# Performance work log

Hardware: AMD Instinct MI355X
Metric: run time of the kernel (lower is better)

The kernel has to match this reference:

```python
import jax, jax.numpy as jnp
import numpy as np

H, HD, ROPE_BASE, E = 16, 64, 10000.0, 8
D, F = 1024, 2048


def layer_norm(x, g, b, eps=1e-5):
    mu = jnp.mean(x, axis=-1, keepdims=True)
    var = jnp.mean((x - mu) ** 2, axis=-1, keepdims=True)
    return (x - mu) * jax.lax.rsqrt(var + eps) * g + b


def apply_rotary(x, cos, sin):
    d = x.shape[-1]
    x1, x2 = x[..., : d // 2], x[..., d // 2:]
    return jnp.concatenate([x1 * cos - x2 * sin, x1 * sin + x2 * cos], axis=-1)


def setup_inputs() -> dict:
    key = jax.random.key(0)
    ks = jax.random.split(key, 8)
    B, T = 2, 2048
    x = jax.random.normal(ks[0], (B, T, D), jnp.float32)
    mask = jnp.triu(jnp.ones((T, T), bool), k=1)[None, None]  # True = masked (causal)
    s = 0.02
    return {
        "x": x,
        "mask": mask,
        "pos_offset": 0,
        "ln1_g": jnp.ones((D,), jnp.float32),
        "ln1_b": jnp.zeros((D,), jnp.float32),
        "qkv_w": jax.random.normal(ks[1], (D, 3 * H * HD), jnp.float32) * s,
        "qkv_b": jnp.zeros((3 * H * HD,), jnp.float32),
        "attn_out_w": jax.random.normal(ks[2], (H * HD, D), jnp.float32) * s,
        "attn_out_b": jnp.zeros((D,), jnp.float32),
        "ln2_g": jnp.ones((D,), jnp.float32),
        "ln2_b": jnp.zeros((D,), jnp.float32),
        "gate_w": jax.random.normal(ks[3], (D, E), jnp.float32) * s,
        "gate_b": jnp.zeros((E,), jnp.float32),
        "fc_w": jax.random.normal(ks[4], (E, D, 2 * F), jnp.float32) * s,
        "fc_b": jnp.zeros((E, 2 * F), jnp.float32),
        "eout_w": jax.random.normal(ks[5], (E, F, D), jnp.float32) * s,
        "eout_b": jnp.zeros((E, D), jnp.float32),
    }


def reference(x, mask, pos_offset, ln1_g, ln1_b, qkv_w, qkv_b, attn_out_w, attn_out_b,
              ln2_g, ln2_b, gate_w, gate_b, fc_w, fc_b, eout_w, eout_b):
    B, T, _ = x.shape
    # ---- Self-attention with inline RoPE ----
    h = layer_norm(x, ln1_g, ln1_b)
    qkv = h @ qkv_w + qkv_b  # [B,T,3*H*HD]
    q, k, v = jnp.split(qkv, 3, axis=-1)
    q, k, v = (t.reshape(B, T, H, HD).transpose(0, 2, 1, 3) for t in (q, k, v))  # [B,H,T,HD]
    inv_freq = 1.0 / ROPE_BASE ** (jnp.arange(0, HD, 2, dtype=jnp.float32) / HD)
    pos = (jnp.arange(T) + pos_offset).astype(jnp.float32)
    freqs = pos[:, None] * inv_freq[None, :]  # [T,HD/2]
    cos, sin = jnp.cos(freqs)[None, None], jnp.sin(freqs)[None, None]
    q = apply_rotary(q, cos, sin)
    k = apply_rotary(k, cos, sin)
    attn = jnp.einsum('bhqd,bhkd->bhqk', q, k) / (HD ** 0.5)
    attn = jnp.where(mask, -jnp.finfo(attn.dtype).max, attn)
    w = jax.nn.softmax(attn, axis=-1)
    o = jnp.einsum('bhqk,bhkd->bhqd', w, v).transpose(0, 2, 1, 3).reshape(B, T, H * HD)
    x = x + (o @ attn_out_w + attn_out_b)
    # ---- Dense soft-MoE GEGLU feed-forward ----
    h2 = layer_norm(x, ln2_g, ln2_b).reshape(-1, D)  # [N,D]
    gate_probs = jax.nn.softmax(h2 @ gate_w + gate_b, axis=-1)  # [N,E]
    fc = jnp.einsum('nd,edf->nef', h2, fc_w) + fc_b  # [N,E,2F]
    x1, x2 = jnp.split(fc, 2, axis=-1)
    act = x1 * jax.nn.gelu(x2, approximate=False)  # [N,E,F]
    expert_out = jnp.einsum('nef,efd->ned', act, eout_w) + eout_b  # [N,E,D]
    weighted = jnp.einsum('ned,ne->nd', expert_out, gate_probs)
    util = jnp.mean(gate_probs, axis=0)
    util_loss = jnp.sum((util - 1.0 / E) ** 2)
    return x + weighted.reshape(B, T, D), util_loss
```

## Files before the change

kernel.cpp:

```cpp
#include <hip/hip_runtime.h>
#include <hip/hip_bf16.h>

typedef __hip_bfloat16 bf16;
typedef short bf16x8 __attribute__((ext_vector_type(8)));
typedef float f32x4 __attribute__((ext_vector_type(4)));

__device__ __forceinline__ unsigned short f2bf(float f){
  __hip_bfloat16 h = __float2bfloat16(f);
  unsigned short u; __builtin_memcpy(&u, &h, 2); return u;
}

__device__ __forceinline__ void gload_lds16(const void* g, void* l){
  __builtin_amdgcn_global_load_lds((const __attribute__((address_space(1))) unsigned int*)g,
                                   (__attribute__((address_space(3))) unsigned int*)l, 16, 0, 0);
}

__device__ __forceinline__ float fast_gelu(float x){
  float t = 1.5957691216f * x * (1.f + 0.044715f * x * x);
  return x / (1.f + __expf(-t));
}


__global__ __launch_bounds__(256) void packT_kernel(const float* __restrict__ in, bf16* __restrict__ out, int R, int C){
  __shared__ float tile[32][33];
  const int tid = threadIdx.x;
  const int tc = tid & 31, tr = tid >> 5;
  const int r0 = blockIdx.y * 32, c0 = blockIdx.x * 32;
  #pragma unroll
  for (int i=0;i<4;i++)
    tile[tr + i*8][tc] = in[(size_t)(r0 + tr + i*8)*C + c0 + tc];
  __syncthreads();
  #pragma unroll
  for (int i=0;i<4;i++){
    int oc = tr + i*8;
    out[(size_t)(c0 + oc)*R + r0 + tc] = __float2bfloat16(tile[tc][oc]);
  }
}

__global__ __launch_bounds__(256) void pack_fc_kernel(const float* __restrict__ fcw, bf16* __restrict__ out){
  __shared__ float tile[32][33];
  const int tid = threadIdx.x;
  const int tc = tid & 31, tr = tid >> 5;
  const int e = blockIdx.z;
  const int d0 = blockIdx.y * 32, j0 = blockIdx.x * 32;
  #pragma unroll
  for (int i=0;i<4;i++)
    tile[tr + i*8][tc] = fcw[((size_t)e*1024 + d0 + tr + i*8)*4096 + j0 + tc];
  __syncthreads();
  #pragma unroll
  for (int i=0;i<4;i++){
    int j = j0 + tr + i*8;
    int cl = ((j & 2047) >> 4)*32 + (j >> 11)*16 + (j & 15);
    out[((size_t)e*4096 + cl)*1024 + d0 + tc] = __float2bfloat16(tile[tc][tr + i*8]);
  }
}

__global__ __launch_bounds__(256) void pack_eout_kernel(const float* __restrict__ eow, bf16* __restrict__ out){
  __shared__ float tile[32][33];
  const int tid = threadIdx.x;
  const int tc = tid & 31, tr = tid >> 5;
  const int e = blockIdx.z;
  const int d0 = blockIdx.y * 32, f0 = blockIdx.x * 32;
  #pragma unroll
  for (int i=0;i<4;i++)
    tile[tr + i*8][tc] = eow[((size_t)e*2048 + f0 + tr + i*8)*1024 + d0 + tc];
  __syncthreads();
  #pragma unroll
  for (int i=0;i<4;i++){
    int d = d0 + tr + i*8;
    out[(size_t)d*16384 + e*2048 + f0 + tc] = __float2bfloat16(tile[tc][tr + i*8]);
  }
}

__global__ __launch_bounds__(256) void pack_biasfc_kernel(const float* __restrict__ fcb, float* __restrict__ biasFc){
  int c = blockIdx.x*256 + threadIdx.x;
  int e = c >> 12, cl = c & 4095;
  int g = cl >> 5, w = cl & 31;
  int j = (w >> 4)*2048 + g*16 + (w & 15);
  biasFc[c] = fcb[e*4096 + j];
}


__global__ __launch_bounds__(256) void ln1_kernel(const float* __restrict__ x, const float* __restrict__ g,
                                                  const float* __restrict__ b, bf16* __restrict__ h){
  const int row = blockIdx.x, tid = threadIdx.x;
  const int lane = tid & 63, wave = tid >> 6;
  const float4 v = reinterpret_cast<const float4*>(x + (size_t)row*1024)[tid];
  float s1 = v.x + v.y + v.z + v.w;
  float s2 = v.x*v.x + v.y*v.y + v.z*v.z + v.w*v.w;
  #pragma unroll
  for (int off=1; off<64; off<<=1){ s1 += __shfl_xor(s1, off); s2 += __shfl_xor(s2, off); }
  __shared__ float rb[8];
  if (lane == 0){ rb[wave] = s1; rb[4+wave] = s2; }
  __syncthreads();
  s1 = rb[0]+rb[1]+rb[2]+rb[3];
  s2 = rb[4]+rb[5]+rb[6]+rb[7];
  const float mu = s1 * (1.f/1024.f);
  const float rst = rsqrtf(s2 * (1.f/1024.f) - mu*mu + 1e-5f);
  const float4 gg = reinterpret_cast<const float4*>(g)[tid];
  const float4 bb = reinterpret_cast<const float4*>(b)[tid];
  ushort4 st;
  st.x = f2bf((v.x-mu)*rst*gg.x + bb.x);
  st.y = f2bf((v.y-mu)*rst*gg.y + bb.y);
  st.z = f2bf((v.z-mu)*rst*gg.z + bb.z);
  st.w = f2bf((v.w-mu)*rst*gg.w + bb.w);
  reinterpret_cast<ushort4*>(h + (size_t)row*1024)[tid] = st;
}

__global__ __launch_bounds__(256) void ln2gate_kernel(const float* __restrict__ xr, const float* __restrict__ g,
    const float* __restrict__ b, const float* __restrict__ gw, const float* __restrict__ gb,
    bf16* __restrict__ h2, float* __restrict__ gate){
  const int row = blockIdx.x, tid = threadIdx.x;
  const int lane = tid & 63, wave = tid >> 6;
  const float4 v = reinterpret_cast<const float4*>(xr + (size_t)row*1024)[tid];
  float s1 = v.x+v.y+v.z+v.w, s2 = v.x*v.x+v.y*v.y+v.z*v.z+v.w*v.w;
  #pragma unroll
  for (int off=1; off<64; off<<=1){ s1 += __shfl_xor(s1, off); s2 += __shfl_xor(s2, off); }
  __shared__ float rb[8];
  if (lane == 0){ rb[wave] = s1; rb[4+wave] = s2; }
  __syncthreads();
  s1 = rb[0]+rb[1]+rb[2]+rb[3];
  s2 = rb[4]+rb[5]+rb[6]+rb[7];
  const float mu = s1*(1.f/1024.f);
  const float rst = rsqrtf(s2*(1.f/1024.f) - mu*mu + 1e-5f);
  const int c = tid*4;
  const float4 gg = reinterpret_cast<const float4*>(g)[tid];
  const float4 bb = reinterpret_cast<const float4*>(b)[tid];
  float nh[4];
  nh[0] = (v.x-mu)*rst*gg.x + bb.x;
  nh[1] = (v.y-mu)*rst*gg.y + bb.y;
  nh[2] = (v.z-mu)*rst*gg.z + bb.z;
  nh[3] = (v.w-mu)*rst*gg.w + bb.w;
  ushort4 st; st.x = f2bf(nh[0]); st.y = f2bf(nh[1]); st.z = f2bf(nh[2]); st.w = f2bf(nh[3]);
  reinterpret_cast<ushort4*>(h2 + (size_t)row*1024)[tid] = st;
  float gp[8];
  #pragma unroll
  for (int e=0;e<8;e++)
    gp[e] = nh[0]*gw[(c+0)*8+e] + nh[1]*gw[(c+1)*8+e] + nh[2]*gw[(c+2)*8+e] + nh[3]*gw[(c+3)*8+e];
  #pragma unroll
  for (int off=1; off<64; off<<=1)
    #pragma unroll
    for (int e=0;e<8;e++) gp[e] += __shfl_xor(gp[e], off);
  __shared__ float gbuf[4][8];
  if (lane == 0)
    #pragma unroll
    for (int e=0;e<8;e++) gbuf[wave][e] = gp[e];
  __syncthreads();
  if (tid == 0){
    float l[8], mx = -1e30f;
    #pragma unroll
    for (int e=0;e<8;e++){ l[e] = gbuf[0][e]+gbuf[1][e]+gbuf[2][e]+gbuf[3][e] + gb[e]; mx = fmaxf(mx, l[e]); }
    float se = 0.f;
    #pragma unroll
    for (int e=0;e<8;e++){ l[e] = __expf(l[e]-mx); se += l[e]; }
    const float inv = 1.f/se;
    #pragma unroll
    for (int e=0;e<8;e++) gate[row*8+e] = l[e]*inv;
  }
}

template<int EPI>
__global__ __launch_bounds__(256) void gemm_bt(
    const bf16* __restrict__ A, const bf16* __restrict__ BT,
    int N, int K, int kPerSlice,
    bf16* __restrict__ outb, float* __restrict__ outf,
    const float* __restrict__ bias, const float* __restrict__ resid,
    const float* __restrict__ gate)
{
  __shared__ __align__(16) bf16 As[128*32];
  __shared__ __align__(16) bf16 Bs[128*32];
  const int tid = threadIdx.x;
  const int lane = tid & 63, wave = tid >> 6;
  const int wr = wave >> 1, wc = wave & 1;
  const int lr = lane & 15, lg = lane >> 4;
  const int row0 = blockIdx.y * 128, col0 = blockIdx.x * 128;
  const int kstart = blockIdx.z * kPerSlice, kend = kstart + kPerSlice;

  const int swzA = lg ^ ((lr >> 1) & 3);

  f32x4 acc[4][4];
  #pragma unroll
  for (int i=0;i<4;i++)
    #pragma unroll
    for (int j=0;j<4;j++) acc[i][j] = (f32x4){0.f,0.f,0.f,0.f};

  for (int k0 = kstart; k0 < kend; k0 += 32){
    if (k0 != kstart) __syncthreads();
    #pragma unroll
    for (int i=0;i<2;i++){
      int ch = i*256 + tid;
      int r = ch >> 2, c = ch & 3;
      int cs = c ^ ((r >> 1) & 3);
      gload_lds16(A  + (size_t)(row0 + r)*K + k0 + cs*8, (void*)&As[ch*8]);
      gload_lds16(BT + (size_t)(col0 + r)*K + k0 + cs*8, (void*)&Bs[ch*8]);
    }
    __syncthreads();
    bf16x8 a[4], bfr[4];
    #pragma unroll
    for (int mi=0;mi<4;mi++) a[mi] = *reinterpret_cast<const bf16x8*>(&As[(wr*64 + mi*16 + lr)*32 + swzA*8]);
    #pragma unroll
    for (int ni=0;ni<4;ni++) bfr[ni] = *reinterpret_cast<const bf16x8*>(&Bs[(wc*64 + ni*16 + lr)*32 + swzA*8]);
    #pragma unroll
    for (int mi=0;mi<4;mi++)
      #pragma unroll
      for (int ni=0;ni<4;ni++)
        acc[mi][ni] = __builtin_amdgcn_mfma_f32_16x16x32_bf16(a[mi], bfr[ni], acc[mi][ni], 0,0,0);
  }

  const int rbase0 = row0 + wr*64;
  #pragma unroll
  for (int mi=0;mi<4;mi++){
    const int r4 = rbase0 + mi*16 + lg*4;
    #pragma unroll
    for (int ni=0;ni<4;ni++){
      const int c = col0 + wc*64 + ni*16 + lr;
      #pragma unroll
      for (int j=0;j<4;j++){
        const int rr = r4 + j;
        float v = acc[mi][ni][j];
        if (EPI == 0) outb[(size_t)rr*N + c] = __float2bfloat16(v + bias[c]);
        else outf[(size_t)rr*N + c] = v + bias[c] + resid[(size_t)rr*N + c];
      }
    }
  }
}

template<int EPI>
__global__ __launch_bounds__(512, 2) void gemm256(
    const bf16* __restrict__ A, const bf16* __restrict__ BT,
    int K, int kPerSlice,
    bf16* __restrict__ outb, float* __restrict__ outf,
    const float* __restrict__ bias, const float* __restrict__ gate)
{
  __shared__ __align__(16) bf16 lds[2][2][16384];
  const int tid = threadIdx.x;
  const int lane = tid & 63, wave = tid >> 6;
  const int wr = wave >> 2, wc = wave & 3;
  const int lr = lane & 15, lg = lane >> 4;
  const int row0 = blockIdx.y * 256, col0 = blockIdx.x * 256;
  const int kstart = blockIdx.z * kPerSlice;
  const int NT = kPerSlice >> 6;
  const int NITER = NT >> 1;

  f32x4 acc[8][4];
  #pragma unroll
  for (int i=0;i<8;i++)
    #pragma unroll
    for (int j=0;j<4;j++) acc[i][j] = (f32x4){0.f,0.f,0.f,0.f};

  auto stage = [&](int t, int ht){
    if (t >= NT) return;
    const bf16* gbase = (ht < 2) ? (A  + (size_t)(row0 + (ht&1)*128) * K)
                                 : (BT + (size_t)(col0 + (ht&1)*128) * K);
    const int k0 = kstart + t*64;
    bf16* dst = &lds[t&1][ht>>1][(ht&1)*8192];
    #pragma unroll
    for (int l=0;l<2;l++){
      const int c = tid + l*512;
      const int r = c >> 3, col16 = c & 7;
      const int cs = col16 ^ (r & 7);
      gload_lds16(gbase + (size_t)r*K + k0 + cs*8, (void*)&dst[c*8]);
    }
  };

  bf16x8 afr[4][2], bfr[4][2];
  auto rdA = [&](int mh, int buf){
    #pragma unroll
    for (int m2=0;m2<4;m2++)
      #pragma unroll
      for (int kk=0;kk<2;kk++){
        const int row = wr*128 + mh*64 + m2*16 + lr;
        afr[m2][kk] = *reinterpret_cast<const bf16x8*>(
            &lds[buf][0][row*64 + (((kk*4+lg) ^ (lr&7))*8)]);
      }
  };
  auto rdB = [&](int nh, int buf){
    #pragma unroll
    for (int n2=0;n2<2;n2++)
      #pragma unroll
      for (int kk=0;kk<2;kk++){
        const int row = wc*64 + (nh*2+n2)*16 + lr;
        bfr[nh*2+n2][kk] = *reinterpret_cast<const bf16x8*>(
            &lds[buf][1][row*64 + (((kk*4+lg) ^ (lr&7))*8)]);
      }
  };
  auto mfmaQ = [&](int mh, int nh){
    __builtin_amdgcn_s_setprio(1);
    #pragma unroll
    for (int m2=0;m2<4;m2++)
      #pragma unroll
      for (int n2=0;n2<2;n2++)
        #pragma unroll
        for (int kk=0;kk<2;kk++)
          acc[mh*4+m2][nh*2+n2] = __builtin_amdgcn_mfma_f32_16x16x32_bf16(
              afr[m2][kk], bfr[nh*2+n2][kk], acc[mh*4+m2][nh*2+n2], 0,0,0);
    __builtin_amdgcn_s_setprio(0);
  };

#define BAR()   __builtin_amdgcn_s_barrier()
#define LGKM0() do { asm volatile("s_waitcnt lgkmcnt(0)" ::: "memory"); \
                     __builtin_amdgcn_sched_barrier(0); } while(0)
#define VMC(n)  do { asm volatile("s_waitcnt vmcnt(" #n ")" ::: "memory"); \
                     __builtin_amdgcn_sched_barrier(0); } while(0)

  stage(0,0); stage(0,1); stage(0,2); stage(0,3); stage(1,0); stage(1,1);
  VMC(4);
  BAR();

  for (int it = 0; it < NITER; ++it){
    const int tB = it*2;
    const bool more = (it + 1 < NITER);

    stage(tB+1, 2); stage(tB+1, 3); rdA(0,0); rdB(0,0);
    LGKM0(); mfmaQ(0,0);
    rdB(1,0);
    LGKM0(); mfmaQ(0,1);
    rdA(1,0);
    LGKM0(); mfmaQ(1,0);
    BAR(); stage(tB+2, 0); stage(tB+2, 1); mfmaQ(1,1);
    if (more) { VMC(4); } else { VMC(0); }
    BAR();

    stage(tB+2, 2); stage(tB+2, 3); rdA(0,1); rdB(0,1);
    LGKM0(); mfmaQ(0,0);
    rdB(1,1);
    LGKM0(); mfmaQ(0,1);
    rdA(1,1);
    LGKM0(); mfmaQ(1,0);
    BAR(); stage(tB+3, 0); stage(tB+3, 1); mfmaQ(1,1);
    if (more) { VMC(4); } else { VMC(0); }
    BAR();
  }
#undef BAR
#undef LGKM0
#undef VMC

  #pragma unroll
  for (int mi=0;mi<8;mi++){
    const int r4 = row0 + wr*128 + mi*16 + lg*4;
    if (EPI == 2){
      #pragma unroll
      for (int p=0;p<2;p++){
        const int c1 = col0 + wc*64 + p*32 + lr;
        const int fg = (c1 >> 5)*16 + lr;
        const int e  = fg >> 11;
        const float b1 = bias[c1], b2 = bias[c1 + 16];
        #pragma unroll
        for (int j=0;j<4;j++){
          const int rr = r4 + j;
          const float x1v = acc[mi][2*p][j] + b1;
          const float x2v = acc[mi][2*p+1][j] + b2;
          const float gl = fast_gelu(x2v);
          outb[(size_t)rr*16384 + fg] = __float2bfloat16(x1v * gl * gate[rr*8 + e]);
        }
      }
    } else {
      #pragma unroll
      for (int ni=0;ni<4;ni++){
        const int c = col0 + wc*64 + ni*16 + lr;
        #pragma unroll
        for (int j=0;j<4;j++)
          outf[(size_t)blockIdx.z*4194304 + (size_t)(r4 + j)*1024 + c] = acc[mi][ni][j];
      }
    }
  }
}

__global__ __launch_bounds__(256) void rope_kernel(bf16* __restrict__ qkv, const int* __restrict__ posoff){
  const int idx = blockIdx.x*256 + threadIdx.x;
  const int i = idx & 31;
  const int h = (idx >> 5) & 15;
  const int n = idx >> 9;
  const float pos = (float)((n & 2047) + posoff[0]);
  const float ang = pos * __expf(-0.2878231366f * (float)i);
  float sn, cs;
  __sincosf(ang, &sn, &cs);
  size_t base = (size_t)n*3072 + h*64 + i;
  {
    float x1 = __bfloat162float(qkv[base]);
    float x2 = __bfloat162float(qkv[base + 32]);
    qkv[base]      = __float2bfloat16((x1*cs - x2*sn) * 0.125f);
    qkv[base + 32] = __float2bfloat16((x1*sn + x2*cs) * 0.125f);
  }
  {
    float x1 = __bfloat162float(qkv[base + 1024]);
    float x2 = __bfloat162float(qkv[base + 1056]);
    qkv[base + 1024] = __float2bfloat16(x1*cs - x2*sn);
    qkv[base + 1056] = __float2bfloat16(x1*sn + x2*cs);
  }
}

__global__ __launch_bounds__(256) void attn_kernel(const bf16* __restrict__ qkv, bf16* __restrict__ o){
  const int bh = blockIdx.y;
  const int b = bh >> 4, h = bh & 15;
  const int tid = threadIdx.x, lane = tid & 63, wave = tid >> 6;
  const int lr = lane & 15, lg = lane >> 4;
  __shared__ __align__(16) bf16 Kt[64*72];
  __shared__ __align__(16) bf16 Vt[64*72];
  __shared__ __align__(16) bf16 P[4][16*72];

  const size_t bbase = (size_t)b*2048*3072;

  bf16x8 kreg[2];
  bf16 vreg[16];

  auto loadKV = [&](int kt){
    #pragma unroll
    for (int i=0;i<2;i++){
      int ch = i*256 + tid;
      int r = ch >> 3, c = ch & 7;
      kreg[i] = *reinterpret_cast<const bf16x8*>(&qkv[bbase + (size_t)(kt*64+r)*3072 + 1024 + h*64 + c*8]);
    }
    #pragma unroll
    for (int i=0;i<16;i++){
      int idx = i*256 + tid;
      int r = idx >> 6, d = idx & 63;
      vreg[i] = qkv[bbase + (size_t)(kt*64+r)*3072 + 2048 + h*64 + d];
    }
  };
  auto writeKV = [&](){
    #pragma unroll
    for (int i=0;i<2;i++){
      int ch = i*256 + tid;
      int r = ch >> 3, c = ch & 7;
      *reinterpret_cast<bf16x8*>(&Kt[r*72 + c*8]) = kreg[i];
    }
    #pragma unroll
    for (int i=0;i<16;i++){
      int idx = i*256 + tid;
      int r = idx >> 6, d = idx & 63;
      Vt[d*72 + r] = vreg[i];
    }
  };

  #pragma unroll 1
  for (int half=0; half<2; half++){
    const int qt = (half == 0) ? (int)blockIdx.x : 31 - (int)blockIdx.x;
    const int qrow = qt*64 + wave*16 + lr;
    bf16x8 qf[2];
    #pragma unroll
    for (int kk=0;kk<2;kk++)
      qf[kk] = *reinterpret_cast<const bf16x8*>(&qkv[bbase + (size_t)qrow*3072 + h*64 + kk*32 + lg*8]);

    f32x4 oacc[4];
    #pragma unroll
    for (int ni=0;ni<4;ni++) oacc[ni] = (f32x4){0.f,0.f,0.f,0.f};
    float mrow[4] = {-1e30f,-1e30f,-1e30f,-1e30f};
    float srow[4] = {0.f,0.f,0.f,0.f};

    loadKV(0);

    #pragma unroll 1
    for (int kt=0; kt<=qt; kt++){
      __syncthreads();
      writeKV();
      __syncthreads();
      if (kt < qt) loadKV(kt+1);

      f32x4 sacc[4];
      #pragma unroll
      for (int ni=0;ni<4;ni++) sacc[ni] = (f32x4){0.f,0.f,0.f,0.f};
      __builtin_amdgcn_s_setprio(1);
      #pragma unroll
      for (int kk=0;kk<2;kk++)
        #pragma unroll
        for (int ni=0;ni<4;ni++){
          bf16x8 kb = *reinterpret_cast<const bf16x8*>(&Kt[(ni*16+lr)*72 + kk*32 + lg*8]);
          sacc[ni] = __builtin_amdgcn_mfma_f32_16x16x32_bf16(qf[kk], kb, sacc[ni], 0,0,0);
        }
      __builtin_amdgcn_s_setprio(0);
      if (kt == qt){
        #pragma unroll
        for (int ni=0;ni<4;ni++)
          #pragma unroll
          for (int j=0;j<4;j++)
            if (ni*16 + lr > wave*16 + lg*4 + j) sacc[ni][j] = -1e30f;
      }
      float pm[4];
      #pragma unroll
      for (int j=0;j<4;j++)
        pm[j] = fmaxf(fmaxf(sacc[0][j], sacc[1][j]), fmaxf(sacc[2][j], sacc[3][j]));
      #pragma unroll
      for (int off=1; off<16; off<<=1)
        #pragma unroll
        for (int j=0;j<4;j++) pm[j] = fmaxf(pm[j], __shfl_xor(pm[j], off));
      float sc[4], rs[4];
      #pragma unroll
      for (int j=0;j<4;j++){
        float mn = fmaxf(mrow[j], pm[j]);
        sc[j] = __expf(mrow[j] - mn);
        mrow[j] = mn;
        rs[j] = 0.f;
      }
      #pragma unroll
      for (int ni=0;ni<4;ni++)
        #pragma unroll
        for (int j=0;j<4;j++){
          float p = __expf(sacc[ni][j] - mrow[j]);
          sacc[ni][j] = p;
          rs[j] += p;
        }
      #pragma unroll
      for (int off=1; off<16; off<<=1)
        #pragma unroll
        for (int j=0;j<4;j++) rs[j] += __shfl_xor(rs[j], off);
      #pragma unroll
      for (int j=0;j<4;j++) srow[j] = srow[j]*sc[j] + rs[j];
      #pragma unroll
      for (int ni=0;ni<4;ni++)
        #pragma unroll
        for (int j=0;j<4;j++)
          P[wave][(lg*4+j)*72 + ni*16 + lr] = __float2bfloat16(sacc[ni][j]);
      #pragma unroll
      for (int ni=0;ni<4;ni++)
        #pragma unroll
        for (int j=0;j<4;j++) oacc[ni][j] *= sc[j];
      asm volatile("s_waitcnt lgkmcnt(0)" ::: "memory");
      __builtin_amdgcn_sched_barrier(0);
      bf16x8 pa0 = *reinterpret_cast<const bf16x8*>(&P[wave][lr*72 + lg*8]);
      bf16x8 pa1 = *reinterpret_cast<const bf16x8*>(&P[wave][lr*72 + 32 + lg*8]);
      __builtin_amdgcn_s_setprio(1);
      #pragma unroll
      for (int ni=0;ni<4;ni++){
        bf16x8 vb0 = *reinterpret_cast<const bf16x8*>(&Vt[(ni*16+lr)*72 + lg*8]);
        oacc[ni] = __builtin_amdgcn_mfma_f32_16x16x32_bf16(pa0, vb0, oacc[ni], 0,0,0);
        bf16x8 vb1 = *reinterpret_cast<const bf16x8*>(&Vt[(ni*16+lr)*72 + 32 + lg*8]);
        oacc[ni] = __builtin_amdgcn_mfma_f32_16x16x32_bf16(pa1, vb1, oacc[ni], 0,0,0);
      }
      __builtin_amdgcn_s_setprio(0);
    }
    #pragma unroll
    for (int ni=0;ni<4;ni++)
      #pragma unroll
      for (int j=0;j<4;j++){
        int row = qt*64 + wave*16 + lg*4 + j;
        int col = h*64 + ni*16 + lr;
        o[(size_t)(b*2048 + row)*1024 + col] = __float2bfloat16(oacc[ni][j] / srow[j]);
      }
  }
}

__global__ __launch_bounds__(256) void reduce_out_kernel(const float* __restrict__ partial, const float* __restrict__ xres,
    const float* __restrict__ gate, const float* __restrict__ eob, float* __restrict__ out){
  const int idx = blockIdx.x*256 + threadIdx.x;
  float4 v = reinterpret_cast<const float4*>(xres)[idx];
  #pragma unroll
  for (int s=0;s<4;s++){
    float4 p = reinterpret_cast<const float4*>(partial + (size_t)s*4194304)[idx];
    v.x += p.x; v.y += p.y; v.z += p.z; v.w += p.w;
  }
  const int n = idx >> 8;
  const int c = (idx << 2) & 1023;
  #pragma unroll
  for (int e=0;e<8;e++){
    const float gp = gate[n*8+e];
    const float4 eb = *reinterpret_cast<const float4*>(&eob[e*1024 + c]);
    v.x += gp*eb.x; v.y += gp*eb.y; v.z += gp*eb.z; v.w += gp*eb.w;
  }
  reinterpret_cast<float4*>(out)[idx] = v;
}

__global__ __launch_bounds__(256) void util_kernel(const float* __restrict__ gate, float* __restrict__ outloss){
  const int tid = threadIdx.x, lane = tid & 63, wave = tid >> 6;
  float p[8] = {0,0,0,0,0,0,0,0};
  for (int r = tid; r < 4096; r += 256)
    #pragma unroll
    for (int e=0;e<8;e++) p[e] += gate[r*8+e];
  #pragma unroll
  for (int off=1; off<64; off<<=1)
    #pragma unroll
    for (int e=0;e<8;e++) p[e] += __shfl_xor(p[e], off);
  __shared__ float rb[4][8];
  if (lane == 0)
    #pragma unroll
    for (int e=0;e<8;e++) rb[wave][e] = p[e];
  __syncthreads();
  if (tid == 0){
    float loss = 0.f;
    #pragma unroll
    for (int e=0;e<8;e++){
      float u = (rb[0][e]+rb[1][e]+rb[2][e]+rb[3][e]) * (1.f/4096.f) - 0.125f;
      loss += u*u;
    }
    outloss[0] = loss;
  }
}

extern "C" void kernel_launch(void* const* d_in, const int* in_sizes, int n_in,
                              void* d_out, int out_size, void* d_ws, size_t ws_size,
                              hipStream_t stream){
  const float* x    = (const float*)d_in[0];
  const int*   poff = (const int*)  d_in[2];
  const float* ln1g = (const float*)d_in[3];
  const float* ln1b = (const float*)d_in[4];
  const float* qkvw = (const float*)d_in[5];
  const float* qkvb = (const float*)d_in[6];
  const float* aow  = (const float*)d_in[7];
  const float* aob  = (const float*)d_in[8];
  const float* ln2g = (const float*)d_in[9];
  const float* ln2b = (const float*)d_in[10];
  const float* gw   = (const float*)d_in[11];
  const float* gb   = (const float*)d_in[12];
  const float* fcw  = (const float*)d_in[13];
  const float* fcb  = (const float*)d_in[14];
  const float* eow  = (const float*)d_in[15];
  const float* eob  = (const float*)d_in[16];
  float* out = (float*)d_out;
  char* ws = (char*)d_ws;

  if (ws_size < 260308992ull) return;

  bf16*  WqkvT  = (bf16*)(ws + 0);
  bf16*  WattnT = (bf16*)(ws + 6291456);
  bf16*  h1     = (bf16*)(ws + 8388608);
  bf16*  qkv    = (bf16*)(ws + 16777216);
  bf16*  o      = (bf16*)(ws + 41943040);
  bf16*  act    = (bf16*)(ws + 0);
  bf16*  WfcT   = (bf16*)(ws + 134217728);
  float* partial= (float*)(ws + 134217728);
  bf16*  WeoutT = (bf16*)(ws + 201326592);
  float* biasFc = (float*)(ws + 234881024);
  float* xres   = (float*)(ws + 235012096);
  bf16*  h2     = (bf16*)(ws + 251789312);
  float* gate   = (float*)(ws + 260177920);

  packT_kernel<<<dim3(96,32), 256, 0, stream>>>(qkvw, WqkvT, 1024, 3072);
  packT_kernel<<<dim3(32,32), 256, 0, stream>>>(aow, WattnT, 1024, 1024);
  pack_fc_kernel<<<dim3(128,32,8), 256, 0, stream>>>(fcw, WfcT);
  pack_eout_kernel<<<dim3(64,32,8), 256, 0, stream>>>(eow, WeoutT);
  pack_biasfc_kernel<<<128, 256, 0, stream>>>(fcb, biasFc);

  ln1_kernel<<<4096, 256, 0, stream>>>(x, ln1g, ln1b, h1);
  gemm_bt<0><<<dim3(24,32), 256, 0, stream>>>(h1, WqkvT, 3072, 1024, 1024, qkv, nullptr, qkvb, nullptr, nullptr);
  rope_kernel<<<8192, 256, 0, stream>>>(qkv, poff);
  attn_kernel<<<dim3(16,32), 256, 0, stream>>>(qkv, o);
  gemm_bt<1><<<dim3(8,32), 256, 0, stream>>>(o, WattnT, 1024, 1024, 1024, nullptr, xres, aob, x, nullptr);
  ln2gate_kernel<<<4096, 256, 0, stream>>>(xres, ln2g, ln2b, gw, gb, h2, gate);
  gemm256<2><<<dim3(128,16), 512, 0, stream>>>(h2, WfcT, 1024, 1024, act, nullptr, biasFc, gate);
  gemm256<4><<<dim3(4,16,4), 512, 0, stream>>>(act, WeoutT, 16384, 4096, nullptr, partial, nullptr, nullptr);
  reduce_out_kernel<<<4096, 256, 0, stream>>>(partial, xres, gate, eob, out);
  util_kernel<<<1, 256, 0, stream>>>(gate, out + 4194304);
}
```

Baseline: 694.8 us.

## Make fc GEMM blocks loop over multiple column tiles with cross-tile prefetch

The fc GEMM (gemm256<2>) now launches 16x16 blocks, each walking 8 consecutive 256-column output tiles. The staging lambda prefetches the next tile's first k-slices of A and B while the current tile's last iterations and epilogue run, so the pipeline is not drained between tiles. The aim is to cut block launch and pipeline fill/drain costs and to reuse the resident A rows. The trade-off is only 256 blocks (one wave on 256 CUs at 2 blocks/CU, leaving half the slots idle) and more complex barrier/waitcnt logic that could be subtly wrong.

```diff
diff --git a/kernel.cpp b/kernel.cpp
--- a/kernel.cpp
+++ b/kernel.cpp
@@ -228,7 +228,7 @@
 template<int EPI>
 __global__ __launch_bounds__(512, 2) void gemm256(
     const bf16* __restrict__ A, const bf16* __restrict__ BT,
-    int K, int kPerSlice,
+    int K, int kPerSlice, int xtiles,
     bf16* __restrict__ outb, float* __restrict__ outf,
     const float* __restrict__ bias, const float* __restrict__ gate)
 {
@@ -237,21 +237,22 @@
   const int lane = tid & 63, wave = tid >> 6;
   const int wr = wave >> 2, wc = wave & 3;
   const int lr = lane & 15, lg = lane >> 4;
-  const int row0 = blockIdx.y * 256, col0 = blockIdx.x * 256;
+  const int row0 = blockIdx.y * 256;
   const int kstart = blockIdx.z * kPerSlice;
   const int NT = kPerSlice >> 6;
   const int NITER = NT >> 1;
+  int col0 = blockIdx.x * xtiles * 256;
 
   f32x4 acc[8][4];
-  #pragma unroll
-  for (int i=0;i<8;i++)
-    #pragma unroll
-    for (int j=0;j<4;j++) acc[i][j] = (f32x4){0.f,0.f,0.f,0.f};
-
-  auto stage = [&](int t, int ht){
-    if (t >= NT) return;
+
+  auto stageT = [&](int T, int ht, bool lastXi){
+    int t = T, col = col0;
+    if (T >= NT){
+      if (lastXi) return;
+      t = T - NT; col = col0 + 256;
+    }
     const bf16* gbase = (ht < 2) ? (A  + (size_t)(row0 + (ht&1)*128) * K)
-                                 : (BT + (size_t)(col0 + (ht&1)*128) * K);
+                                 : (BT + (size_t)(col  + (ht&1)*128) * K);
     const int k0 = kstart + t*64;
     bf16* dst = &lds[t&1][ht>>1][(ht&1)*8192];
     #pragma unroll
@@ -303,67 +304,79 @@
 #define VMC(n)  do { asm volatile("s_waitcnt vmcnt(" #n ")" ::: "memory"); \
                      __builtin_amdgcn_sched_barrier(0); } while(0)
 
-  stage(0,0); stage(0,1); stage(0,2); stage(0,3); stage(1,0); stage(1,1);
+  stageT(0,0,false); stageT(0,1,false); stageT(0,2,false); stageT(0,3,false);
+  stageT(1,0,false); stageT(1,1,false);
   VMC(4);
   BAR();
 
-  for (int it = 0; it < NITER; ++it){
-    const int tB = it*2;
-    const bool more = (it + 1 < NITER);
-
-    stage(tB+1, 2); stage(tB+1, 3); rdA(0,0); rdB(0,0);
-    LGKM0(); mfmaQ(0,0);
-    rdB(1,0);
-    LGKM0(); mfmaQ(0,1);
-    rdA(1,0);
-    LGKM0(); mfmaQ(1,0);
-    BAR(); stage(tB+2, 0); stage(tB+2, 1); mfmaQ(1,1);
-    if (more) { VMC(4); } else { VMC(0); }
-    BAR();
-
-    stage(tB+2, 2); stage(tB+2, 3); rdA(0,1); rdB(0,1);
-    LGKM0(); mfmaQ(0,0);
-    rdB(1,1);
-    LGKM0(); mfmaQ(0,1);
-    rdA(1,1);
-    LGKM0(); mfmaQ(1,0);
-    BAR(); stage(tB+3, 0); stage(tB+3, 1); mfmaQ(1,1);
-    if (more) { VMC(4); } else { VMC(0); }
-    BAR();
+  for (int xi = 0; xi < xtiles; ++xi){
+    col0 = (blockIdx.x * xtiles + xi) * 256;
+    const bool lx = (xi == xtiles - 1);
+
+    #pragma unroll
+    for (int i=0;i<8;i++)
+      #pragma unroll
+      for (int j=0;j<4;j++) acc[i][j] = (f32x4){0.f,0.f,0.f,0.f};
+
+    for (int it = 0; it < NITER; ++it){
+      const int tB = it*2;
+      const bool tailIter = lx && (it + 1 == NITER);
+
+      stageT(tB+1, 2, lx); stageT(tB+1, 3, lx); rdA(0,0); rdB(0,0);
+      LGKM0(); mfmaQ(0,0);
+      rdB(1,0);
+      LGKM0(); mfmaQ(0,1);
+      rdA(1,0);
+      LGKM0(); mfmaQ(1,0);
+      BAR(); stageT(tB+2, 0, lx); stageT(tB+2, 1, lx); mfmaQ(1,1);
+      if (tailIter) { VMC(0); } else { VMC(4); }
+      BAR();
+
+      stageT(tB+2, 2, lx); stageT(tB+2, 3, lx); rdA(0,1); rdB(0,1);
+      LGKM0(); mfmaQ(0,0);
+      rdB(1,1);
+      LGKM0(); mfmaQ(0,1);
+      rdA(1,1);
+      LGKM0(); mfmaQ(1,0);
+      BAR(); stageT(tB+3, 0, lx); stageT(tB+3, 1, lx); mfmaQ(1,1);
+      if (it + 1 < NITER) { VMC(4); BAR(); }
+    }
+
+    #pragma unroll
+    for (int mi=0;mi<8;mi++){
+      const int r4 = row0 + wr*128 + mi*16 + lg*4;
+      if (EPI == 2){
+        #pragma unroll
+        for (int p=0;p<2;p++){
+          const int c1 = col0 + wc*64 + p*32 + lr;
+          const int fg = (c1 >> 5)*16 + lr;
+          const int e  = fg >> 11;
+          const float b1 = bias[c1], b2 = bias[c1 + 16];
+          #pragma unroll
+          for (int j=0;j<4;j++){
+            const int rr = r4 + j;
+            const float x1v = acc[mi][2*p][j] + b1;
+            const float x2v = acc[mi][2*p+1][j] + b2;
+            const float gl = fast_gelu(x2v);
+            outb[(size_t)rr*16384 + fg] = __float2bfloat16(x1v * gl * gate[rr*8 + e]);
+          }
+        }
+      } else {
+        #pragma unroll
+        for (int ni=0;ni<4;ni++){
+          const int c = col0 + wc*64 + ni*16 + lr;
+          #pragma unroll
+          for (int j=0;j<4;j++)
+            outf[(size_t)blockIdx.z*4194304 + (size_t)(r4 + j)*1024 + c] = acc[mi][ni][j];
+        }
+      }
+    }
+
+    if (!lx){ VMC(4); BAR(); }
   }
 #undef BAR
 #undef LGKM0
 #undef VMC
-
-  #pragma unroll
-  for (int mi=0;mi<8;mi++){
-    const int r4 = row0 + wr*128 + mi*16 + lg*4;
-    if (EPI == 2){
-      #pragma unroll
-      for (int p=0;p<2;p++){
-        const int c1 = col0 + wc*64 + p*32 + lr;
-        const int fg = (c1 >> 5)*16 + lr;
-        const int e  = fg >> 11;
-        const float b1 = bias[c1], b2 = bias[c1 + 16];
-        #pragma unroll
-        for (int j=0;j<4;j++){
-          const int rr = r4 + j;
-          const float x1v = acc[mi][2*p][j] + b1;
-          const float x2v = acc[mi][2*p+1][j] + b2;
-          const float gl = fast_gelu(x2v);
-          outb[(size_t)rr*16384 + fg] = __float2bfloat16(x1v * gl * gate[rr*8 + e]);
-        }
-      }
-    } else {
-      #pragma unroll
-      for (int ni=0;ni<4;ni++){
-        const int c = col0 + wc*64 + ni*16 + lr;
-        #pragma unroll
-        for (int j=0;j<4;j++)
-          outf[(size_t)blockIdx.z*4194304 + (size_t)(r4 + j)*1024 + c] = acc[mi][ni][j];
-      }
-    }
-  }
 }
 
 __global__ __launch_bounds__(256) void rope_kernel(bf16* __restrict__ qkv, const int* __restrict__ posoff){
@@ -636,8 +649,8 @@
   attn_kernel<<<dim3(16,32), 256, 0, stream>>>(qkv, o);
   gemm_bt<1><<<dim3(8,32), 256, 0, stream>>>(o, WattnT, 1024, 1024, 1024, nullptr, xres, aob, x, nullptr);
   ln2gate_kernel<<<4096, 256, 0, stream>>>(xres, ln2g, ln2b, gw, gb, h2, gate);
-  gemm256<2><<<dim3(128,16), 512, 0, stream>>>(h2, WfcT, 1024, 1024, act, nullptr, biasFc, gate);
-  gemm256<4><<<dim3(4,16,4), 512, 0, stream>>>(act, WeoutT, 16384, 4096, nullptr, partial, nullptr, nullptr);
+  gemm256<2><<<dim3(16,16), 512, 0, stream>>>(h2, WfcT, 1024, 1024, 8, act, nullptr, biasFc, gate);
+  gemm256<4><<<dim3(4,16,4), 512, 0, stream>>>(act, WeoutT, 16384, 4096, 1, nullptr, partial, nullptr, nullptr);
   reduce_out_kernel<<<4096, 256, 0, stream>>>(partial, xres, gate, eob, out);
   util_kernel<<<1, 256, 0, stream>>>(gate, out + 4194304);
 }
```

Measured after the change: 818.4 us. 17.8% more time.
